# Optimization experiments

Hardware: AMD Instinct MI355X
Metric: run time of the kernel (lower is better)

## Reference

```python
import jax, jax.numpy as jnp
import numpy as np
import math

N, D, C = 1024, 512, 70722
M_MARGIN = 0.4
H_SCALE = 0.333
S_SCALE = 64.0
EPS = 0.001


def setup_inputs() -> dict:
    key = jax.random.key(0)
    k1, k2, k3 = jax.random.split(key, 3)
    x = jax.random.normal(k1, (N, D), dtype=jnp.float32)
    labels = jax.random.randint(k2, (N,), 0, C, dtype=jnp.int64)
    # weights ~ N(0, 0.01) as in nn.Parameter init
    weights = 0.01 * jax.random.normal(k3, (C, D), dtype=jnp.float32)
    return {"x": x, "labels": labels, "weights": weights}


def reference(x, labels, weights):
    # world_size == 1: all-gather is identity and all labels are local.
    x_norms = jnp.maximum(jnp.linalg.norm(x, axis=1, keepdims=True), 1e-8)  # [N,1]

    norm_emb = x / jnp.maximum(jnp.linalg.norm(x, axis=1, keepdims=True), 1e-12)
    norm_w = weights / jnp.maximum(jnp.linalg.norm(weights, axis=1, keepdims=True), 1e-12)
    cosine = jnp.clip(norm_emb @ norm_w.T, -1.0, 1.0)  # [N,C]

    # AdaFace adaptive margin scaler (detached norms; t_alpha=1 -> batch stats = current stats)
    safe_norms = jax.lax.stop_gradient(jnp.clip(x_norms, 0.001, 100.0))  # [N,1]
    batch_mean = jnp.mean(safe_norms)
    batch_std = jnp.std(safe_norms, ddof=1)  # torch .std() is unbiased
    margin_scaler = jnp.clip((safe_norms - batch_mean) / (batch_std + EPS) * H_SCALE, -1.0, 1.0)  # [N,1]

    g_angular = -M_MARGIN * margin_scaler           # [N,1]
    g_add = M_MARGIN + M_MARGIN * margin_scaler     # [N,1]

    onehot = jax.nn.one_hot(labels, C, dtype=cosine.dtype)  # [N,C]

    theta = jnp.arccos(cosine)
    theta_m = jnp.clip(theta + onehot * g_angular, EPS, math.pi - EPS)
    logits = (jnp.cos(theta_m) - onehot * g_add) * S_SCALE  # [N,C]

    logp = jax.nn.log_softmax(logits, axis=-1)
    loss = -jnp.mean(jnp.take_along_axis(logp, labels[:, None], axis=1))
    return loss
```

## Files before the change

### kernel.cpp

```cpp
#include <hip/hip_runtime.h>
#include <hip/hip_bf16.h>
#include <stdint.h>

#define DIM 512
#define NROWS 1024
#define NCLS 70722
#define NC16 4421

typedef float floatx4 __attribute__((ext_vector_type(4)));

__device__ __forceinline__ unsigned pk4_fp8(float a, float b, float c, float d) {
    unsigned v = 0;
    v = __builtin_amdgcn_cvt_pk_fp8_f32(a, b, v, false);
    v = __builtin_amdgcn_cvt_pk_fp8_f32(c, d, v, true);
    return v;
}

__device__ __forceinline__ float wave_reduce_sum(float s) {
    #pragma unroll
    for (int m = 1; m < 64; m <<= 1) s += __shfl_xor(s, m);
    return s;
}

__global__ __launch_bounds__(256) void prep_kernel(
        const float* __restrict__ x, const float* __restrict__ W,
        const int* __restrict__ labels,
        uint8_t* __restrict__ AnT, uint8_t* __restrict__ WT,
        float* __restrict__ rownorm, float* __restrict__ coslab,
        float* __restrict__ rowsum) {
    int b = blockIdx.x;
    int wv = threadIdx.x >> 6, lane = threadIdx.x & 63;
    if (b < NROWS / 4) {
        if (threadIdx.x < 4) rowsum[b * 4 + threadIdx.x] = 0.0f;
        int row = b * 4 + wv;
        int lab = labels[row];
        const float4* xs = (const float4*)(x + (size_t)row * DIM);
        const float4* ws = (const float4*)(W + (size_t)lab * DIM);
        float4 xa = xs[lane * 2], xb = xs[lane * 2 + 1];
        float4 wa = ws[lane * 2], wb = ws[lane * 2 + 1];
        float dxx = xa.x*xa.x + xa.y*xa.y + xa.z*xa.z + xa.w*xa.w
                  + xb.x*xb.x + xb.y*xb.y + xb.z*xb.z + xb.w*xb.w;
        float dww = wa.x*wa.x + wa.y*wa.y + wa.z*wa.z + wa.w*wa.w
                  + wb.x*wb.x + wb.y*wb.y + wb.z*wb.z + wb.w*wb.w;
        float dxw = xa.x*wa.x + xa.y*wa.y + xa.z*wa.z + xa.w*wa.w
                  + xb.x*wb.x + xb.y*wb.y + xb.z*wb.z + xb.w*wb.w;
        dxx = wave_reduce_sum(dxx);
        dww = wave_reduce_sum(dww);
        dxw = wave_reduce_sum(dxw);
        float norm = sqrtf(dxx);
        float s16 = 16.0f / fmaxf(norm, 1e-12f);
        uint2 p;
        p.x = pk4_fp8(xa.x*s16, xa.y*s16, xa.z*s16, xa.w*s16);
        p.y = pk4_fp8(xb.x*s16, xb.y*s16, xb.z*s16, xb.w*s16);
        *(uint2*)(AnT + (size_t)(row >> 4) * 8192 + lane * 128 + (row & 15) * 8) = p;
        if (lane == 0) {
            rownorm[row] = norm;
            coslab[row]  = dxw / (fmaxf(norm, 1e-12f) * fmaxf(sqrtf(dww), 1e-12f));
        }
    } else {
        int g = (b - NROWS / 4) * 4 + wv;
        if (g < NC16) {
            uint2 p[16];
            #pragma unroll
            for (int i = 0; i < 16; ++i) {
                int c = g * 16 + i;
                float4 va = {0.f, 0.f, 0.f, 0.f}, vb = {0.f, 0.f, 0.f, 0.f};
                if (c < NCLS) {
                    const float4* src = (const float4*)(W + (size_t)c * DIM);
                    va = src[lane * 2]; vb = src[lane * 2 + 1];
                }
                float ss = va.x*va.x + va.y*va.y + va.z*va.z + va.w*va.w
                         + vb.x*vb.x + vb.y*vb.y + vb.z*vb.z + vb.w*vb.w;
                ss = wave_reduce_sum(ss);
                float s16 = 16.0f / fmaxf(sqrtf(ss), 1e-12f);
                p[i].x = pk4_fp8(va.x*s16, va.y*s16, va.z*s16, va.w*s16);
                p[i].y = pk4_fp8(vb.x*s16, vb.y*s16, vb.z*s16, vb.w*s16);
            }
            uint8_t* dst = WT + (size_t)g * 8192 + lane * 128;
            #pragma unroll
            for (int j = 0; j < 8; ++j) {
                uint4 q;
                q.x = p[2*j].x;   q.y = p[2*j].y;
                q.z = p[2*j+1].x; q.w = p[2*j+1].y;
                *(uint4*)(dst + j * 16) = q;
            }
        }
    }
}

__global__ __launch_bounds__(512) void gemm8_kernel(
        const uint8_t* __restrict__ AnT, const uint8_t* __restrict__ WT,
        float* __restrict__ rowsum) {
    __shared__ float red[128];
    int b = blockIdx.x;
    int mgrp = b >> 5, cgrp = b & 31;
    int tid = threadIdx.x, lane = tid & 63, wv = tid >> 6;

    int wm = (wv >> 2) * 64, wn = (wv & 3) * 64;
    int fr = lane & 15, fq = lane >> 4;

    long af[4][16];
    const uint8_t* ab = AnT + (size_t)(mgrp * 8 + (wm >> 4)) * 8192 + fq * 128 + fr * 8;
    #pragma unroll
    for (int m = 0; m < 4; ++m)
        #pragma unroll
        for (int ksl = 0; ksl < 16; ++ksl)
            af[m][ksl] = *(const long*)(ab + m * 8192 + ksl * 512);

    if (tid < 128) red[tid] = 0.0f;
    __syncthreads();

    const floatx4 vzero = {0.0f, 0.0f, 0.0f, 0.0f};
    floatx4 acc[4][4] = {};

    int nct = (cgrp < 21) ? 9 : 8;
    int c = cgrp;
    for (int ct = 0; ct < nct; ++ct) {
        const uint8_t* bb[4];
        #pragma unroll
        for (int n = 0; n < 4; ++n) {
            int g = min(c * 16 + (wn >> 4) + n, NC16 - 1);
            bb[n] = WT + (size_t)g * 8192 + fq * 128 + fr * 8;
        }
        #pragma unroll
        for (int kb = 0; kb < 4; ++kb) {
            long bg[4][4];
            #pragma unroll
            for (int n = 0; n < 4; ++n)
                #pragma unroll
                for (int ks = 0; ks < 4; ++ks)
                    bg[n][ks] = *(const long*)(bb[n] + kb * 2048 + ks * 512);
            __builtin_amdgcn_s_setprio(1);
            #pragma unroll
            for (int ks = 0; ks < 4; ++ks)
                #pragma unroll
                for (int m = 0; m < 4; ++m)
                    #pragma unroll
                    for (int n = 0; n < 4; ++n)
                        acc[m][n] = __builtin_amdgcn_mfma_f32_16x16x32_fp8_fp8(
                            af[m][kb * 4 + ks], bg[n][ks], acc[m][n], 0, 0, 0);
            __builtin_amdgcn_s_setprio(0);
        }

        {
            const float CLIPC = 0.99999950f;
            const float ISCL  = 1.0f / 256.0f;
            int colbase = c * 256 + wn + fr;
            #pragma unroll
            for (int m = 0; m < 4; ++m) {
                #pragma unroll
                for (int reg = 0; reg < 4; ++reg) {
                    float s = 0.0f;
                    #pragma unroll
                    for (int n = 0; n < 4; ++n) {
                        int col = colbase + n * 16;
                        float cc = acc[m][n][reg] * ISCL;
                        cc = fminf(fmaxf(cc, -CLIPC), CLIPC);
                        float term = __expf(64.0f * cc - 64.0f);
                        s += (col < NCLS) ? term : 0.0f;
                    }
                    s += __shfl_xor(s, 1); s += __shfl_xor(s, 2);
                    s += __shfl_xor(s, 4); s += __shfl_xor(s, 8);
                    if (fr == 0) atomicAdd(&red[wm + m * 16 + fq * 4 + reg], s);
                }
            }
            #pragma unroll
            for (int m = 0; m < 4; ++m)
                #pragma unroll
                for (int n = 0; n < 4; ++n)
                    acc[m][n] = vzero;
        }
        c += 32;
    }

    __syncthreads();
    if (tid < 128) atomicAdd(rowsum + mgrp * 128 + tid, red[tid]);
}

__global__ __launch_bounds__(1024) void finalize_kernel(
        const float* __restrict__ rowsum, const float* __restrict__ coslab,
        const float* __restrict__ rownorm, float* __restrict__ out) {
    __shared__ float part[16];
    __shared__ float bc[2];
    int t = threadIdx.x, lane = t & 63, w = t >> 6;
    float v = fminf(fmaxf(rownorm[t], 0.001f), 100.0f);

    float s = wave_reduce_sum(v);
    if (lane == 0) part[w] = s;
    __syncthreads();
    if (t < 64) {
        float p = (lane < 16) ? part[lane] : 0.0f;
        p = wave_reduce_sum(p);
        if (lane == 0) bc[0] = p * (1.0f / 1024.0f);
    }
    __syncthreads();
    float mean = bc[0];
    float d = v - mean;

    s = wave_reduce_sum(d * d);
    if (lane == 0) part[w] = s;
    __syncthreads();
    if (t < 64) {
        float p = (lane < 16) ? part[lane] : 0.0f;
        p = wave_reduce_sum(p);
        if (lane == 0) bc[1] = sqrtf(p * (1.0f / 1023.0f));
    }
    __syncthreads();
    float stdv = bc[1];

    float ms = d / (stdv + 0.001f) * 0.333f;
    ms = fminf(fmaxf(ms, -1.0f), 1.0f);
    float g_ang = -0.4f * ms;
    float g_add =  0.4f + 0.4f * ms;
    const float CLIPC = 0.99999950f;
    const float PI = 3.14159265358979323846f;
    float cl  = fminf(fmaxf(coslab[t], -1.0f), 1.0f);
    float cne = fminf(fmaxf(cl, -CLIPC), CLIPC);
    float logit_non = 64.0f * cne;
    float theta = acosf(cl);
    float tm = fminf(fmaxf(theta + g_ang, 0.001f), PI - 0.001f);
    float logit_true = (__cosf(tm) - g_add) * 64.0f;
    float ssum = rowsum[t] - __expf(logit_non - 64.0f) + __expf(logit_true - 64.0f);
    float loss = logf(ssum) + 64.0f - logit_true;

    s = wave_reduce_sum(loss);
    if (lane == 0) part[w] = s;
    __syncthreads();
    if (t < 64) {
        float p = (lane < 16) ? part[lane] : 0.0f;
        p = wave_reduce_sum(p);
        if (lane == 0) out[0] = p * (1.0f / 1024.0f);
    }
}

extern "C" void kernel_launch(void* const* d_in, const int* in_sizes, int n_in,
                              void* d_out, int out_size, void* d_ws, size_t ws_size,
                              hipStream_t stream) {
    const float* x      = (const float*)d_in[0];
    const int*   labels = (const int*)d_in[1];
    const float* W      = (const float*)d_in[2];
    float* out = (float*)d_out;
    char* ws = (char*)d_ws;

    const size_t SZ_WT = (size_t)NC16 * 8192;
    const size_t SZ_AN = 524288;
    uint8_t* WT  = (uint8_t*)ws;
    uint8_t* AnT = (uint8_t*)(ws + SZ_WT);
    float* rownorm = (float*)(ws + SZ_WT + SZ_AN);
    float* rowsum  = rownorm + 1024;
    float* coslab  = rowsum + 1024;

    int wblocks = (NC16 + 3) / 4;
    prep_kernel<<<NROWS / 4 + wblocks, 256, 0, stream>>>(
        x, W, labels, AnT, WT, rownorm, coslab, rowsum);
    gemm8_kernel<<<256, 512, 0, stream>>>(AnT, WT, rowsum);
    finalize_kernel<<<1, 1024, 0, stream>>>(rowsum, coslab, rownorm, out);
}
```

Before: 295.8 us.

## Double-buffer B loads in fp8 GEMM, fuse finalize, restructure weight prep via LDS

The GEMM loop now prefetches the next K-slice of weight fragments into a second register set while MFMAs run on the current one, and it prefetches across column tiles. The finalize kernel is folded into the GEMM through a last-block-done atomic counter, which removes one launch. The weight prep now gives each block one 16-class group spread over four waves and transposes through LDS for coalesced 32-byte stores, instead of one wave per group doing 16 serial row reductions. Risks are higher register pressure from the doubled B buffers combined with the launch_bounds minimum of 2 blocks, plus correctness that depends on the threadfence/atomic pattern.

New measurement: 373.6 us. 1.26x slower.

```diff
diff --git a/kernel.cpp b/kernel.cpp
--- a/kernel.cpp
+++ b/kernel.cpp
@@ -27,10 +27,12 @@
         const int* __restrict__ labels,
         uint8_t* __restrict__ AnT, uint8_t* __restrict__ WT,
         float* __restrict__ rownorm, float* __restrict__ coslab,
-        float* __restrict__ rowsum) {
+        float* __restrict__ rowsum, int* __restrict__ done) {
+    __shared__ uint8_t lds[16 * 520];
     int b = blockIdx.x;
     int wv = threadIdx.x >> 6, lane = threadIdx.x & 63;
     if (b < NROWS / 4) {
+        if (b == 0 && threadIdx.x == 0) *done = 0;
         if (threadIdx.x < 4) rowsum[b * 4 + threadIdx.x] = 0.0f;
         int row = b * 4 + wv;
         int lab = labels[row];
@@ -58,40 +60,54 @@
             coslab[row]  = dxw / (fmaxf(norm, 1e-12f) * fmaxf(sqrtf(dww), 1e-12f));
         }
     } else {
-        int g = (b - NROWS / 4) * 4 + wv;
-        if (g < NC16) {
-            uint2 p[16];
-            #pragma unroll
-            for (int i = 0; i < 16; ++i) {
-                int c = g * 16 + i;
-                float4 va = {0.f, 0.f, 0.f, 0.f}, vb = {0.f, 0.f, 0.f, 0.f};
-                if (c < NCLS) {
-                    const float4* src = (const float4*)(W + (size_t)c * DIM);
-                    va = src[lane * 2]; vb = src[lane * 2 + 1];
-                }
-                float ss = va.x*va.x + va.y*va.y + va.z*va.z + va.w*va.w
-                         + vb.x*vb.x + vb.y*vb.y + vb.z*vb.z + vb.w*vb.w;
-                ss = wave_reduce_sum(ss);
-                float s16 = 16.0f / fmaxf(sqrtf(ss), 1e-12f);
-                p[i].x = pk4_fp8(va.x*s16, va.y*s16, va.z*s16, va.w*s16);
-                p[i].y = pk4_fp8(vb.x*s16, vb.y*s16, vb.z*s16, vb.w*s16);
+        int g = b - NROWS / 4;
+        float4 va[4], vb[4];
+        #pragma unroll
+        for (int j = 0; j < 4; ++j) {
+            int c = g * 16 + wv * 4 + j;
+            va[j] = make_float4(0.f, 0.f, 0.f, 0.f);
+            vb[j] = make_float4(0.f, 0.f, 0.f, 0.f);
+            if (c < NCLS) {
+                const float4* src = (const float4*)(W + (size_t)c * DIM);
+                va[j] = src[lane * 2]; vb[j] = src[lane * 2 + 1];
             }
-            uint8_t* dst = WT + (size_t)g * 8192 + lane * 128;
-            #pragma unroll
-            for (int j = 0; j < 8; ++j) {
-                uint4 q;
-                q.x = p[2*j].x;   q.y = p[2*j].y;
-                q.z = p[2*j+1].x; q.w = p[2*j+1].y;
-                *(uint4*)(dst + j * 16) = q;
-            }
-        }
-    }
-}
-
-__global__ __launch_bounds__(512) void gemm8_kernel(
+        }
+        #pragma unroll
+        for (int j = 0; j < 4; ++j) {
+            float ss = va[j].x*va[j].x + va[j].y*va[j].y + va[j].z*va[j].z + va[j].w*va[j].w
+                     + vb[j].x*vb[j].x + vb[j].y*vb[j].y + vb[j].z*vb[j].z + vb[j].w*vb[j].w;
+            ss = wave_reduce_sum(ss);
+            float s16 = 16.0f / fmaxf(sqrtf(ss), 1e-12f);
+            uint2 p;
+            p.x = pk4_fp8(va[j].x*s16, va[j].y*s16, va[j].z*s16, va[j].w*s16);
+            p.y = pk4_fp8(vb[j].x*s16, vb[j].y*s16, vb[j].z*s16, vb[j].w*s16);
+            int r = wv * 4 + j;
+            *(uint2*)(&lds[r * 520 + lane * 8]) = p;
+        }
+        __syncthreads();
+        int t = threadIdx.x;
+        uint2 v0 = *(const uint2*)&lds[((4*t+0) & 15) * 520 + ((4*t+0) >> 4) * 8];
+        uint2 v1 = *(const uint2*)&lds[((4*t+1) & 15) * 520 + ((4*t+1) >> 4) * 8];
+        uint2 v2 = *(const uint2*)&lds[((4*t+2) & 15) * 520 + ((4*t+2) >> 4) * 8];
+        uint2 v3 = *(const uint2*)&lds[((4*t+3) & 15) * 520 + ((4*t+3) >> 4) * 8];
+        uint4 q0, q1;
+        q0.x = v0.x; q0.y = v0.y; q0.z = v1.x; q0.w = v1.y;
+        q1.x = v2.x; q1.y = v2.y; q1.z = v3.x; q1.w = v3.y;
+        uint8_t* dst = WT + (size_t)g * 8192 + t * 32;
+        *(uint4*)dst        = q0;
+        *(uint4*)(dst + 16) = q1;
+    }
+}
+
+__global__ __launch_bounds__(512, 2) void gemm8_kernel(
         const uint8_t* __restrict__ AnT, const uint8_t* __restrict__ WT,
-        float* __restrict__ rowsum) {
+        float* __restrict__ rowsum, const float* __restrict__ coslab,
+        const float* __restrict__ rownorm, float* __restrict__ out,
+        int* __restrict__ done) {
     __shared__ float red[128];
+    __shared__ float fpart[8];
+    __shared__ float fbc[2];
+    __shared__ int lastBlk;
     int b = blockIdx.x;
     int mgrp = b >> 5, cgrp = b & 31;
     int tid = threadIdx.x, lane = tid & 63, wv = tid >> 6;
@@ -112,35 +128,47 @@
 
     const floatx4 vzero = {0.0f, 0.0f, 0.0f, 0.0f};
     floatx4 acc[4][4] = {};
+    long bgA[4][4], bgB[4][4];
+    const uint8_t* bb[4];
+
+#define SETBB(cc) do { \
+        _Pragma("unroll") \
+        for (int n = 0; n < 4; ++n) { \
+            int g = min((cc) * 16 + (wn >> 4) + n, NC16 - 1); \
+            bb[n] = WT + (size_t)g * 8192 + fq * 128 + fr * 8; \
+        } } while (0)
+
+#define LOADBG(BG, kb) do { \
+        _Pragma("unroll") \
+        for (int n = 0; n < 4; ++n) \
+            _Pragma("unroll") \
+            for (int ks = 0; ks < 4; ++ks) \
+                BG[n][ks] = *(const long*)(bb[n] + (kb) * 2048 + ks * 512); \
+    } while (0)
+
+#define MFMA64(kb, BG) do { \
+        __builtin_amdgcn_s_setprio(1); \
+        _Pragma("unroll") \
+        for (int ks = 0; ks < 4; ++ks) \
+            _Pragma("unroll") \
+            for (int m = 0; m < 4; ++m) \
+                _Pragma("unroll") \
+                for (int n = 0; n < 4; ++n) \
+                    acc[m][n] = __builtin_amdgcn_mfma_f32_16x16x32_fp8_fp8( \
+                        af[m][(kb) * 4 + ks], BG[n][ks], acc[m][n], 0, 0, 0); \
+        __builtin_amdgcn_s_setprio(0); \
+    } while (0)
 
     int nct = (cgrp < 21) ? 9 : 8;
     int c = cgrp;
+    SETBB(c);
+    LOADBG(bgA, 0);
     for (int ct = 0; ct < nct; ++ct) {
-        const uint8_t* bb[4];
-        #pragma unroll
-        for (int n = 0; n < 4; ++n) {
-            int g = min(c * 16 + (wn >> 4) + n, NC16 - 1);
-            bb[n] = WT + (size_t)g * 8192 + fq * 128 + fr * 8;
-        }
-        #pragma unroll
-        for (int kb = 0; kb < 4; ++kb) {
-            long bg[4][4];
-            #pragma unroll
-            for (int n = 0; n < 4; ++n)
-                #pragma unroll
-                for (int ks = 0; ks < 4; ++ks)
-                    bg[n][ks] = *(const long*)(bb[n] + kb * 2048 + ks * 512);
-            __builtin_amdgcn_s_setprio(1);
-            #pragma unroll
-            for (int ks = 0; ks < 4; ++ks)
-                #pragma unroll
-                for (int m = 0; m < 4; ++m)
-                    #pragma unroll
-                    for (int n = 0; n < 4; ++n)
-                        acc[m][n] = __builtin_amdgcn_mfma_f32_16x16x32_fp8_fp8(
-                            af[m][kb * 4 + ks], bg[n][ks], acc[m][n], 0, 0, 0);
-            __builtin_amdgcn_s_setprio(0);
-        }
+        LOADBG(bgB, 1);  MFMA64(0, bgA);
+        LOADBG(bgA, 2);  MFMA64(1, bgB);
+        LOADBG(bgB, 3);  MFMA64(2, bgA);
+        if (ct < nct - 1) { SETBB(c + 32); LOADBG(bgA, 0); }
+        MFMA64(3, bgB);
 
         {
             const float CLIPC = 0.99999950f;
@@ -172,62 +200,72 @@
         }
         c += 32;
     }
+#undef SETBB
+#undef LOADBG
+#undef MFMA64
 
     __syncthreads();
     if (tid < 128) atomicAdd(rowsum + mgrp * 128 + tid, red[tid]);
-}
-
-__global__ __launch_bounds__(1024) void finalize_kernel(
-        const float* __restrict__ rowsum, const float* __restrict__ coslab,
-        const float* __restrict__ rownorm, float* __restrict__ out) {
-    __shared__ float part[16];
-    __shared__ float bc[2];
-    int t = threadIdx.x, lane = t & 63, w = t >> 6;
-    float v = fminf(fmaxf(rownorm[t], 0.001f), 100.0f);
-
-    float s = wave_reduce_sum(v);
-    if (lane == 0) part[w] = s;
-    __syncthreads();
-    if (t < 64) {
-        float p = (lane < 16) ? part[lane] : 0.0f;
+    __syncthreads();
+    if (tid == 0) {
+        __threadfence();
+        int old = atomicAdd(done, 1);
+        lastBlk = (old == 255);
+    }
+    __syncthreads();
+    if (!lastBlk) return;
+
+    float v0 = fminf(fmaxf(rownorm[tid],       0.001f), 100.0f);
+    float v1 = fminf(fmaxf(rownorm[tid + 512], 0.001f), 100.0f);
+    float s = wave_reduce_sum(v0 + v1);
+    if (lane == 0) fpart[wv] = s;
+    __syncthreads();
+    if (tid < 64) {
+        float p = (lane < 8) ? fpart[lane] : 0.0f;
         p = wave_reduce_sum(p);
-        if (lane == 0) bc[0] = p * (1.0f / 1024.0f);
-    }
-    __syncthreads();
-    float mean = bc[0];
-    float d = v - mean;
-
-    s = wave_reduce_sum(d * d);
-    if (lane == 0) part[w] = s;
-    __syncthreads();
-    if (t < 64) {
-        float p = (lane < 16) ? part[lane] : 0.0f;
+        if (lane == 0) fbc[0] = p * (1.0f / 1024.0f);
+    }
+    __syncthreads();
+    float mean = fbc[0];
+    float d0 = v0 - mean, d1 = v1 - mean;
+    s = wave_reduce_sum(d0 * d0 + d1 * d1);
+    if (lane == 0) fpart[wv] = s;
+    __syncthreads();
+    if (tid < 64) {
+        float p = (lane < 8) ? fpart[lane] : 0.0f;
         p = wave_reduce_sum(p);
-        if (lane == 0) bc[1] = sqrtf(p * (1.0f / 1023.0f));
-    }
-    __syncthreads();
-    float stdv = bc[1];
-
-    float ms = d / (stdv + 0.001f) * 0.333f;
-    ms = fminf(fmaxf(ms, -1.0f), 1.0f);
-    float g_ang = -0.4f * ms;
-    float g_add =  0.4f + 0.4f * ms;
+        if (lane == 0) fbc[1] = sqrtf(p * (1.0f / 1023.0f));
+    }
+    __syncthreads();
+    float stdv = fbc[1];
+
     const float CLIPC = 0.99999950f;
     const float PI = 3.14159265358979323846f;
-    float cl  = fminf(fmaxf(coslab[t], -1.0f), 1.0f);
-    float cne = fminf(fmaxf(cl, -CLIPC), CLIPC);
-    float logit_non = 64.0f * cne;
-    float theta = acosf(cl);
-    float tm = fminf(fmaxf(theta + g_ang, 0.001f), PI - 0.001f);
-    float logit_true = (__cosf(tm) - g_add) * 64.0f;
-    float ssum = rowsum[t] - __expf(logit_non - 64.0f) + __expf(logit_true - 64.0f);
-    float loss = logf(ssum) + 64.0f - logit_true;
-
-    s = wave_reduce_sum(loss);
-    if (lane == 0) part[w] = s;
-    __syncthreads();
-    if (t < 64) {
-        float p = (lane < 16) ? part[lane] : 0.0f;
+    float lsum = 0.0f;
+    #pragma unroll
+    for (int h = 0; h < 2; ++h) {
+        int r = tid + h * 512;
+        float d = (h == 0) ? d0 : d1;
+        float ms = d / (stdv + 0.001f) * 0.333f;
+        ms = fminf(fmaxf(ms, -1.0f), 1.0f);
+        float g_ang = -0.4f * ms;
+        float g_add =  0.4f + 0.4f * ms;
+        float cl  = fminf(fmaxf(coslab[r], -1.0f), 1.0f);
+        float cne = fminf(fmaxf(cl, -CLIPC), CLIPC);
+        float logit_non = 64.0f * cne;
+        float theta = acosf(cl);
+        float tm = fminf(fmaxf(theta + g_ang, 0.001f), PI - 0.001f);
+        float logit_true = (__cosf(tm) - g_add) * 64.0f;
+        float rs = __hip_atomic_load(&rowsum[r], __ATOMIC_RELAXED,
+                                     __HIP_MEMORY_SCOPE_AGENT);
+        float ssum = rs - __expf(logit_non - 64.0f) + __expf(logit_true - 64.0f);
+        lsum += logf(ssum) + 64.0f - logit_true;
+    }
+    s = wave_reduce_sum(lsum);
+    if (lane == 0) fpart[wv] = s;
+    __syncthreads();
+    if (tid < 64) {
+        float p = (lane < 8) ? fpart[lane] : 0.0f;
         p = wave_reduce_sum(p);
         if (lane == 0) out[0] = p * (1.0f / 1024.0f);
     }
@@ -249,10 +287,10 @@
     float* rownorm = (float*)(ws + SZ_WT + SZ_AN);
     float* rowsum  = rownorm + 1024;
     float* coslab  = rowsum + 1024;
-
-    int wblocks = (NC16 + 3) / 4;
-    prep_kernel<<<NROWS / 4 + wblocks, 256, 0, stream>>>(
-        x, W, labels, AnT, WT, rownorm, coslab, rowsum);
-    gemm8_kernel<<<256, 512, 0, stream>>>(AnT, WT, rowsum);
-    finalize_kernel<<<1, 1024, 0, stream>>>(rowsum, coslab, rownorm, out);
-}
+    int*   done    = (int*)(coslab + 1024);
+
+    prep_kernel<<<NROWS / 4 + NC16, 256, 0, stream>>>(
+        x, W, labels, AnT, WT, rownorm, coslab, rowsum, done);
+    gemm8_kernel<<<256, 512, 0, stream>>>(
+        AnT, WT, rowsum, coslab, rownorm, out, done);
+}
```
